# Optimization experiments

Measured on AMD Instinct MI355X. Metric: run time of the kernel, lower is better.

## Reference

```python
import jax, jax.numpy as jnp
import numpy as np

NUM_CLASSES = 10
MAX_V = 81  # max_width * max_height = 9*9


def _ln(x, w, eps=1e-5):
    # torch LayerNorm with bias=False (weight only)
    m = jnp.mean(x, axis=-1, keepdims=True)
    v = jnp.var(x, axis=-1, keepdims=True)
    return (x - m) / jnp.sqrt(v + eps) * w


def _mha(q_in, k_in, v_in, in_proj, out_proj, nhead):
    # torch nn.MultiheadAttention, bias=False
    d = q_in.shape[-1]
    Wq, Wk, Wv = in_proj[:d], in_proj[d:2 * d], in_proj[2 * d:]
    q = q_in @ Wq.T
    k = k_in @ Wk.T
    v = v_in @ Wv.T
    B, Lq, _ = q.shape
    Lk = k.shape[1]
    hd = d // nhead
    q = q.reshape(B, Lq, nhead, hd)
    k = k.reshape(B, Lk, nhead, hd)
    v = v.reshape(B, Lk, nhead, hd)
    scores = jnp.einsum('bqhd,bkhd->bhqk', q, k) / jnp.sqrt(jnp.asarray(hd, q.dtype))
    attn = jax.nn.softmax(scores, axis=-1)
    o = jnp.einsum('bhqk,bkhd->bqhd', attn, v).reshape(B, Lq, d)
    return o @ out_proj.T


def setup_inputs() -> dict:
    key = jax.random.key(0)
    ks = jax.random.split(key, 16)
    N, C, H, W = 16, NUM_CLASSES, 30, 30
    d = C + 1  # 11
    V = 32

    def rn(k, shape, s=0.2):
        return (jax.random.normal(k, shape) * s).astype(jnp.float32)

    return {
        'x': jax.random.normal(ks[0], (N, C, H, W), dtype=jnp.float32),
        'V_feature': rn(ks[1], (C, V), 1.0),
        'enc_in_proj': rn(ks[2], (3 * d, d)),
        'enc_out_proj': rn(ks[3], (d, d)),
        'enc_lin1': rn(ks[4], (1, d)),
        'enc_lin2': rn(ks[5], (d, 1)),
        'enc_ln1': jnp.ones((d,), jnp.float32),
        'enc_ln2': jnp.ones((d,), jnp.float32),
        'ffV_w': rn(ks[6], (V, MAX_V)),
        'dec_sa_in': rn(ks[7], (3 * V, V)),
        'dec_sa_out': rn(ks[8], (V, V)),
        'dec_ca_in': rn(ks[9], (3 * V, V)),
        'dec_ca_out': rn(ks[10], (V, V)),
        'dec_lin1': rn(ks[11], (1, V)),
        'dec_lin2': rn(ks[12], (V, 1)),
        'dec_ln1': jnp.ones((V,), jnp.float32),
        'dec_ln2': jnp.ones((V,), jnp.float32),
        'dec_ln3': jnp.ones((V,), jnp.float32),
        'W_d0': rn(ks[13], (8, V)),
        'W_d1': rn(ks[14], (1, 8)),
    }


def reference(x, V_feature, enc_in_proj, enc_out_proj, enc_lin1, enc_lin2,
              enc_ln1, enc_ln2, ffV_w, dec_sa_in, dec_sa_out, dec_ca_in,
              dec_ca_out, dec_lin1, dec_lin2, dec_ln1, dec_ln2, dec_ln3,
              W_d0, W_d1):
    N, C, H, W = x.shape
    # PixelVectorExtractor: pad(0) + all-ones channel padded with 1, 3x3 unfold
    xp = jnp.pad(x, ((0, 0), (0, 0), (1, 1), (1, 1)))
    ones = jnp.ones((N, 1, H + 2, W + 2), x.dtype)
    xc = jnp.concatenate([xp, ones], axis=1)  # [N, C+1, H+2, W+2]
    # row-major 3x3 patch order matches torch unfold(0,3,1).unfold(1,3,1)
    patches = jnp.stack([xc[:, :, di:di + H, dj:dj + W]
                         for di in range(3) for dj in range(3)], axis=-1)
    feat = patches.transpose(0, 2, 3, 1, 4).reshape(N * H * W, C + 1, 9)
    feat = jnp.pad(feat, ((0, 0), (0, 0), (0, MAX_V - 9)))  # [B, C+1, 81]

    # TransformerEncoder (1 layer, post-norm, nhead=1, relu FF, no dropout)
    f = feat.transpose(0, 2, 1)  # [B, 81, C+1]
    f = _ln(f + _mha(f, f, f, enc_in_proj, enc_out_proj, 1), enc_ln1)
    f = _ln(f + jax.nn.relu(f @ enc_lin1.T) @ enc_lin2.T, enc_ln2)
    f = f.transpose(0, 2, 1)  # [B, C+1, 81]

    mem = f @ ffV_w.T  # ff_V: Linear(81 -> 32, no bias) -> [B, C+1, 32]
    B, _, V = mem.shape

    # TransformerDecoder (1 layer, post-norm, nhead=32 so head_dim=1)
    y = jnp.broadcast_to(V_feature, (B, C, V))
    y = _ln(y + _mha(y, y, y, dec_sa_in, dec_sa_out, V), dec_ln1)
    y = _ln(y + _mha(y, mem, mem, dec_ca_in, dec_ca_out, V), dec_ln2)
    y = _ln(y + jax.nn.relu(y @ dec_lin1.T) @ dec_lin2.T, dec_ln3)

    # decode MLP: 32 -> 8 -> 1
    y = jax.nn.relu(y @ W_d0.T) @ W_d1.T  # [B, C, 1]
    return y.reshape(N, H, W, C).transpose(0, 3, 1, 2)
```

## Files before the change

### kernel.cpp

```cpp
#include <hip/hip_runtime.h>
#include <math.h>


__device__ __forceinline__ float gsum32(float v) {
#pragma unroll
  for (int m = 16; m > 0; m >>= 1) v += __shfl_xor(v, m, 32);
  return v;
}

__device__ __forceinline__ void wsync() {
  asm volatile("s_waitcnt lgkmcnt(0)" ::: "memory");
}

__global__ __launch_bounds__(256) void precompute_kernel(
    const float* __restrict__ Vf,
    const float* __restrict__ enc_in,
    const float* __restrict__ enc_outw,
    const float* __restrict__ ffV_w,
    const float* __restrict__ dec_sa_in,
    const float* __restrict__ dec_sa_out,
    const float* __restrict__ dec_ln1,
    const float* __restrict__ dec_ca_in,
    float* __restrict__ M_enc, float* __restrict__ WVO,
    float* __restrict__ G_k, float* __restrict__ G_v,
    float* __restrict__ y1, float* __restrict__ qca)
{
  const int tid = threadIdx.x;

  if (blockIdx.x == 0) {
    const float rs11 = 0.3015113445777636f;
    for (int idx = tid; idx < 121; idx += 256) {
      int c = idx / 11, cp = idx - c * 11;
      float sm = 0.f, sv = 0.f;
      for (int i = 0; i < 11; ++i) {
        sm += enc_in[i * 11 + c] * enc_in[(11 + i) * 11 + cp];
        sv += enc_outw[c * 11 + i] * enc_in[(22 + i) * 11 + cp];
      }
      M_enc[idx] = sm * rs11;
      WVO[idx] = sv;
    }

    __shared__ float Fsh[320];
    for (int idx = tid; idx < 288; idx += 256) {
      int t = idx >> 5, j = idx & 31;
      Fsh[idx] = ffV_w[j * 81 + t];
    }
    if (tid < 32) {
      float s = 0.f;
      for (int t = 9; t < 81; ++t) s += ffV_w[tid * 81 + t];
      Fsh[288 + tid] = s;
    }
    __syncthreads();

    for (int idx = tid; idx < 640; idx += 256) {
      int which = idx >= 320;
      int r = idx - 320 * which;
      int t = r >> 5, h = r & 31;
      const float* w = dec_ca_in + ((which ? 64 : 32) + h) * 32;
      float s = 0.f;
      for (int j = 0; j < 32; ++j) s += Fsh[t * 32 + j] * w[j];
      (which ? G_v : G_k)[r] = s;
    }
  } else {
    __shared__ float qsa[320], ksa[320], vsa[320], osa[320], zb[320];
    __shared__ float mu[16], rstd[16];

    for (int idx = tid; idx < 960; idx += 256) {
      int m = idx / 320, r = idx - m * 320;
      int t = r >> 5, h = r & 31;
      const float* w = dec_sa_in + (m * 32 + h) * 32;
      const float* yr = Vf + t * 32;
      float s = 0.f;
#pragma unroll
      for (int j = 0; j < 32; ++j) s += yr[j] * w[j];
      (m == 0 ? qsa : m == 1 ? ksa : vsa)[r] = s;
    }
    __syncthreads();

    for (int idx = tid; idx < 320; idx += 256) {
      int h = idx & 31;
      float q = qsa[idx];
      float sc[10];
      float mx = -1e30f;
#pragma unroll
      for (int s = 0; s < 10; ++s) { sc[s] = q * ksa[s * 32 + h]; mx = fmaxf(mx, sc[s]); }
      float den = 0.f, acc = 0.f;
#pragma unroll
      for (int s = 0; s < 10; ++s) {
        float e = __expf(sc[s] - mx);
        den += e;
        acc += e * vsa[s * 32 + h];
      }
      osa[idx] = acc / den;
    }
    __syncthreads();

    for (int idx = tid; idx < 320; idx += 256) {
      int t = idx >> 5, c = idx & 31;
      float s = 0.f;
#pragma unroll
      for (int h = 0; h < 32; ++h) s += osa[t * 32 + h] * dec_sa_out[c * 32 + h];
      zb[idx] = Vf[idx] + s;
    }
    __syncthreads();

    if (tid < 10) {
      float s1 = 0.f, s2 = 0.f;
      for (int c = 0; c < 32; ++c) { float z = zb[tid * 32 + c]; s1 += z; s2 += z * z; }
      float m = s1 * (1.f / 32.f);
      mu[tid] = m;
      rstd[tid] = 1.f / sqrtf(s2 * (1.f / 32.f) - m * m + 1e-5f);
    }
    __syncthreads();

    for (int idx = tid; idx < 320; idx += 256) {
      int t = idx >> 5, c = idx & 31;
      float v = (zb[idx] - mu[t]) * rstd[t] * dec_ln1[c];
      y1[idx] = v;
      zb[idx] = v;
    }
    __syncthreads();

    for (int idx = tid; idx < 320; idx += 256) {
      int t = idx >> 5, h = idx & 31;
      const float* w = dec_ca_in + h * 32;
      float s = 0.f;
#pragma unroll
      for (int j = 0; j < 32; ++j) s += zb[t * 32 + j] * w[j];
      qca[idx] = s;
    }
  }
}

#define SLICE 1376

__global__ __launch_bounds__(256) void pixel_main_kernel(
    const float* __restrict__ x,
    const float* __restrict__ M_enc, const float* __restrict__ WVO,
    const float* __restrict__ enc_lin1, const float* __restrict__ enc_lin2,
    const float* __restrict__ enc_ln1, const float* __restrict__ enc_ln2,
    const float* __restrict__ G_k, const float* __restrict__ G_v,
    const float* __restrict__ y1g, const float* __restrict__ qcag,
    const float* __restrict__ dec_ca_out,
    const float* __restrict__ dec_lin1, const float* __restrict__ dec_lin2,
    const float* __restrict__ dec_ln2v, const float* __restrict__ dec_ln3v,
    const float* __restrict__ W_d0, const float* __restrict__ W_d1,
    float* __restrict__ out)
{
  __shared__ __align__(16) float sh[4 * SLICE];
  const int wave = threadIdx.x >> 6;
  const int lane = threadIdx.x & 63;
  float* ls = sh + wave * SLICE;
  const int F9 = 0, G = 112, VO = 224, SC = 336, ZR = 432, FE = 544, KC = 656, VC = 1008;
  const int OC = 0, ZB = 320;

  const int p = blockIdx.x * 4 + wave;
  const int n = p / 900;
  const int rem = p - n * 900;
  const int pi = rem / 30, pj = rem - (rem / 30) * 30;

  for (int idx = lane; idx < 99; idx += 64) {
    int t = idx / 11, c = idx - t * 11;
    float val = 1.0f;
    if (c < 10) {
      int di = t / 3, dj = t - (t / 3) * 3;
      int ii = pi + di - 1, jj = pj + dj - 1;
      val = (ii >= 0 && ii < 30 && jj >= 0 && jj < 30)
                ? x[((n * 10 + c) * 30 + ii) * 30 + jj] : 0.0f;
    }
    ls[F9 + idx] = val;
  }
  wsync();

  for (int idx = lane; idx < 99; idx += 64) {
    int s = idx / 11, c = idx - (idx / 11) * 11;
    const float* Mr = M_enc + c * 11;
    const float* Wr = WVO + c * 11;
    float ag = 0.f, av = 0.f;
#pragma unroll
    for (int cp = 0; cp < 11; ++cp) {
      float fv = ls[F9 + s * 11 + cp];
      ag += Mr[cp] * fv;
      av += Wr[cp] * fv;
    }
    ls[G + idx] = ag;
    ls[VO + idx] = av;
  }
  wsync();

  for (int idx = lane; idx < 81; idx += 64) {
    int t = idx / 9, s = idx - (idx / 9) * 9;
    float a = 0.f;
#pragma unroll
    for (int c = 0; c < 11; ++c) a += ls[F9 + t * 11 + c] * ls[G + s * 11 + c];
    ls[SC + idx] = a;
  }
  wsync();

  if (lane < 9) {
    float e[9];
    float mx = 0.0f;
#pragma unroll
    for (int s = 0; s < 9; ++s) { e[s] = ls[SC + lane * 9 + s]; mx = fmaxf(mx, e[s]); }
    float den = 72.0f * __expf(-mx);
#pragma unroll
    for (int s = 0; s < 9; ++s) {
      e[s] = __expf(e[s] - mx);
      den += e[s];
      ls[SC + lane * 9 + s] = e[s];
    }
    ls[SC + 81 + lane] = 1.0f / den;
  }
  wsync();

  for (int idx = lane; idx < 110; idx += 64) {
    int t = idx / 11, c = idx - (idx / 11) * 11;
    float a = 0.f;
    if (t < 9) {
#pragma unroll
      for (int s = 0; s < 9; ++s) a += ls[SC + t * 9 + s] * ls[VO + s * 11 + c];
      a = a * ls[SC + 81 + t] + ls[F9 + idx];
    } else {
#pragma unroll
      for (int s = 0; s < 9; ++s) a += ls[VO + s * 11 + c];
      a *= (1.0f / 81.0f);
    }
    ls[ZR + idx] = a;
  }
  wsync();

  if (lane < 10) {
    float row[11];
#pragma unroll
    for (int c = 0; c < 11; ++c) row[c] = ls[ZR + lane * 11 + c];
    float s1 = 0.f, s2 = 0.f;
#pragma unroll
    for (int c = 0; c < 11; ++c) { s1 += row[c]; s2 += row[c] * row[c]; }
    float mu = s1 * (1.0f / 11.0f);
    float rs = 1.0f / sqrtf(s2 * (1.0f / 11.0f) - mu * mu + 1e-5f);
    float h = 0.f;
#pragma unroll
    for (int c = 0; c < 11; ++c) {
      row[c] = (row[c] - mu) * rs * enc_ln1[c];
      h += row[c] * enc_lin1[c];
    }
    h = fmaxf(h, 0.f);
    float t1 = 0.f, t2 = 0.f;
#pragma unroll
    for (int c = 0; c < 11; ++c) {
      row[c] += h * enc_lin2[c];
      t1 += row[c]; t2 += row[c] * row[c];
    }
    float mu2 = t1 * (1.0f / 11.0f);
    float rs2 = 1.0f / sqrtf(t2 * (1.0f / 11.0f) - mu2 * mu2 + 1e-5f);
#pragma unroll
    for (int c = 0; c < 11; ++c)
      ls[FE + lane * 11 + c] = (row[c] - mu2) * rs2 * enc_ln2[c];
  }
  wsync();

  {
    const int h = lane & 31, grp = lane >> 5;
    const float* Gb = grp ? G_v : G_k;
    const int dst = grp ? VC : KC;
    float gr[10];
#pragma unroll
    for (int t = 0; t < 10; ++t) gr[t] = Gb[t * 32 + h];
#pragma unroll
    for (int c = 0; c < 11; ++c) {
      float a = 0.f;
#pragma unroll
      for (int t = 0; t < 10; ++t) a += ls[FE + t * 11 + c] * gr[t];
      ls[dst + c * 32 + h] = a;
    }
  }
  wsync();

  for (int it = 0; it < 5; ++it) {
    int idx = it * 64 + lane;
    int t = idx >> 5, h = idx & 31;
    float q = qcag[t * 32 + h];
    float kreg[11];
#pragma unroll
    for (int s = 0; s < 11; ++s) kreg[s] = q * ls[KC + s * 32 + h];
    float mx = kreg[0];
#pragma unroll
    for (int s = 1; s < 11; ++s) mx = fmaxf(mx, kreg[s]);
    float den = 0.f, acc = 0.f;
#pragma unroll
    for (int s = 0; s < 11; ++s) {
      float e = __expf(kreg[s] - mx);
      den += e;
      acc += e * ls[VC + s * 32 + h];
    }
    ls[OC + idx] = acc / den;
  }
  wsync();

  for (int k = 0; k < 5; ++k) {
    int t = 2 * k + (lane >> 5);
    int c = lane & 31;
    float zacc = 0.f;
    const float4* wrow = (const float4*)(dec_ca_out + c * 32);
    const float4* orow = (const float4*)(ls + OC + t * 32);
#pragma unroll
    for (int h4 = 0; h4 < 8; ++h4) {
      float4 o4 = orow[h4];
      float4 w4 = wrow[h4];
      zacc += o4.x * w4.x + o4.y * w4.y + o4.z * w4.z + o4.w * w4.w;
    }
    float z = y1g[t * 32 + c] + zacc;
    {
      float s1 = gsum32(z), s2 = gsum32(z * z);
      float mu = s1 * (1.0f / 32.0f);
      z = (z - mu) * (1.0f / sqrtf(s2 * (1.0f / 32.0f) - mu * mu + 1e-5f)) * dec_ln2v[c];
    }
    {
      float d1 = gsum32(z * dec_lin1[c]);
      z += fmaxf(d1, 0.f) * dec_lin2[c];
    }
    {
      float s1 = gsum32(z), s2 = gsum32(z * z);
      float mu = s1 * (1.0f / 32.0f);
      z = (z - mu) * (1.0f / sqrtf(s2 * (1.0f / 32.0f) - mu * mu + 1e-5f)) * dec_ln3v[c];
    }
    ls[ZB + t * 32 + c] = z;
  }
  wsync();

  for (int idx = lane; idx < 80; idx += 64) {
    int t = idx >> 3, m = idx & 7;
    const float4* arow = (const float4*)(W_d0 + m * 32);
    const float4* zrow4 = (const float4*)(ls + ZB + t * 32);
    float d = 0.f;
#pragma unroll
    for (int q4 = 0; q4 < 8; ++q4) {
      float4 a4 = arow[q4];
      float4 z4 = zrow4[q4];
      d += a4.x * z4.x + a4.y * z4.y + a4.z * z4.z + a4.w * z4.w;
    }
    ls[OC + idx] = fmaxf(d, 0.f);
  }
  wsync();

  if (lane < 10) {
    float r = 0.f;
#pragma unroll
    for (int m = 0; m < 8; ++m) r += ls[OC + lane * 8 + m] * W_d1[m];
    out[((n * 10 + lane) * 30 + pi) * 30 + pj] = r;
  }
}

extern "C" void kernel_launch(void* const* d_in, const int* in_sizes, int n_in,
                              void* d_out, int out_size, void* d_ws, size_t ws_size,
                              hipStream_t stream) {
  (void)in_sizes; (void)n_in; (void)out_size; (void)ws_size;
  const float* x          = (const float*)d_in[0];
  const float* Vf         = (const float*)d_in[1];
  const float* enc_in     = (const float*)d_in[2];
  const float* enc_outw   = (const float*)d_in[3];
  const float* enc_lin1   = (const float*)d_in[4];
  const float* enc_lin2   = (const float*)d_in[5];
  const float* enc_ln1    = (const float*)d_in[6];
  const float* enc_ln2    = (const float*)d_in[7];
  const float* ffV_w      = (const float*)d_in[8];
  const float* dec_sa_in  = (const float*)d_in[9];
  const float* dec_sa_out = (const float*)d_in[10];
  const float* dec_ca_in  = (const float*)d_in[11];
  const float* dec_ca_out = (const float*)d_in[12];
  const float* dec_lin1   = (const float*)d_in[13];
  const float* dec_lin2   = (const float*)d_in[14];
  const float* dec_ln1    = (const float*)d_in[15];
  const float* dec_ln2    = (const float*)d_in[16];
  const float* dec_ln3    = (const float*)d_in[17];
  const float* W_d0       = (const float*)d_in[18];
  const float* W_d1       = (const float*)d_in[19];
  float* out = (float*)d_out;

  float* ws    = (float*)d_ws;
  float* M_enc = ws;
  float* WVO   = ws + 128;
  float* G_k   = ws + 256;
  float* G_v   = ws + 576;
  float* y1    = ws + 896;
  float* qca   = ws + 1216;

  hipLaunchKernelGGL(precompute_kernel, dim3(2), dim3(256), 0, stream,
                     Vf, enc_in, enc_outw, ffV_w, dec_sa_in, dec_sa_out,
                     dec_ln1, dec_ca_in, M_enc, WVO, G_k, G_v, y1, qca);

  hipLaunchKernelGGL(pixel_main_kernel, dim3(3600), dim3(256), 0, stream,
                     x, M_enc, WVO, enc_lin1, enc_lin2, enc_ln1, enc_ln2,
                     G_k, G_v, y1, qca, dec_ca_out, dec_lin1, dec_lin2,
                     dec_ln2, dec_ln3, W_d0, W_d1, out);
}
```

Before: 171.5 us.

## Keep cross-attention K/V in registers and transpose encoder features in LDS

Encoder output features are now stored in LDS transposed (channel-major, stride 12), so each lane reads its 10 token values with float4 loads. The projected K and V values stay in registers and are exchanged between the two half-waves with a shuffle, instead of going through LDS. Each lane then computes softmax over its own K/V registers. This removes one LDS round trip and a sync, and halves the per-wave LDS slice, which may allow more blocks to be resident. The cost is higher register pressure and broadcast-style float4 LDS reads.

```diff
diff --git a/kernel.cpp b/kernel.cpp
--- a/kernel.cpp
+++ b/kernel.cpp
@@ -132,7 +132,7 @@
   }
 }
 
-#define SLICE 1376
+#define SLICE 704
 
 __global__ __launch_bounds__(256) void pixel_main_kernel(
     const float* __restrict__ x,
@@ -151,7 +151,7 @@
   const int wave = threadIdx.x >> 6;
   const int lane = threadIdx.x & 63;
   float* ls = sh + wave * SLICE;
-  const int F9 = 0, G = 112, VO = 224, SC = 336, ZR = 432, FE = 544, KC = 656, VC = 1008;
+  const int F9 = 0, G = 112, VO = 224, SC = 336, ZR = 432, FET = 544;
   const int OC = 0, ZB = 320;
 
   const int p = blockIdx.x * 4 + wave;
@@ -255,51 +255,59 @@
     float rs2 = 1.0f / sqrtf(t2 * (1.0f / 11.0f) - mu2 * mu2 + 1e-5f);
 #pragma unroll
     for (int c = 0; c < 11; ++c)
-      ls[FE + lane * 11 + c] = (row[c] - mu2) * rs2 * enc_ln2[c];
-  }
-  wsync();
-
+      ls[FET + c * 12 + lane] = (row[c] - mu2) * rs2 * enc_ln2[c];
+  }
+  wsync();
+
+  const int hh = lane & 31, grp = lane >> 5;
+  float kv[11];
   {
-    const int h = lane & 31, grp = lane >> 5;
     const float* Gb = grp ? G_v : G_k;
-    const int dst = grp ? VC : KC;
     float gr[10];
 #pragma unroll
-    for (int t = 0; t < 10; ++t) gr[t] = Gb[t * 32 + h];
-#pragma unroll
-    for (int c = 0; c < 11; ++c) {
-      float a = 0.f;
-#pragma unroll
-      for (int t = 0; t < 10; ++t) a += ls[FE + t * 11 + c] * gr[t];
-      ls[dst + c * 32 + h] = a;
-    }
-  }
-  wsync();
-
-  for (int it = 0; it < 5; ++it) {
-    int idx = it * 64 + lane;
-    int t = idx >> 5, h = idx & 31;
-    float q = qcag[t * 32 + h];
-    float kreg[11];
-#pragma unroll
-    for (int s = 0; s < 11; ++s) kreg[s] = q * ls[KC + s * 32 + h];
-    float mx = kreg[0];
-#pragma unroll
-    for (int s = 1; s < 11; ++s) mx = fmaxf(mx, kreg[s]);
+    for (int t = 0; t < 10; ++t) gr[t] = Gb[t * 32 + hh];
+#pragma unroll
+    for (int cc = 0; cc < 11; ++cc) {
+      const float4* fr = (const float4*)(ls + FET + cc * 12);
+      float4 a = fr[0], b4 = fr[1], c4 = fr[2];
+      float fe[10] = {a.x, a.y, a.z, a.w, b4.x, b4.y, b4.z, b4.w, c4.x, c4.y};
+      float s = 0.f;
+#pragma unroll
+      for (int t = 0; t < 10; ++t) s += fe[t] * gr[t];
+      kv[cc] = s;
+    }
+  }
+  float kk[11], vv[11];
+#pragma unroll
+  for (int cc = 0; cc < 11; ++cc) {
+    float o = __shfl_xor(kv[cc], 32);
+    kk[cc] = grp ? o : kv[cc];
+    vv[cc] = grp ? kv[cc] : o;
+  }
+
+#pragma unroll
+  for (int i = 0; i < 5; ++i) {
+    int t = grp * 5 + i;
+    float q = qcag[t * 32 + hh];
+    float sc[11];
+    float mx = q * kk[0];
+    sc[0] = mx;
+#pragma unroll
+    for (int s = 1; s < 11; ++s) { sc[s] = q * kk[s]; mx = fmaxf(mx, sc[s]); }
     float den = 0.f, acc = 0.f;
 #pragma unroll
     for (int s = 0; s < 11; ++s) {
-      float e = __expf(kreg[s] - mx);
+      float e = __expf(sc[s] - mx);
       den += e;
-      acc += e * ls[VC + s * 32 + h];
-    }
-    ls[OC + idx] = acc / den;
+      acc += e * vv[s];
+    }
+    ls[OC + t * 32 + hh] = acc / den;
   }
   wsync();
 
   for (int k = 0; k < 5; ++k) {
-    int t = 2 * k + (lane >> 5);
-    int c = lane & 31;
+    int t = 2 * k + grp;
+    int c = hh;
     float zacc = 0.f;
     const float4* wrow = (const float4*)(dec_ca_out + c * 32);
     const float4* orow = (const float4*)(ls + OC + t * 32);
```

Measured after the change: 171.1 us. No clear change (-0.3%).
